# Kernel optimization log

Measured on AMD Instinct MI355X. Metric: run time of the kernel, lower is better.

## Reference

```python
import jax, jax.numpy as jnp
import numpy as np
import math

LEVEL_DIMS = [256, 512, 1024, 2048]
B, P, K, D = 8192, 64, 8, 512
EPS = 1e-5  # torch LayerNorm default eps


def _layernorm(x, g, b):
    m = jnp.mean(x, axis=-1, keepdims=True)
    v = jnp.var(x, axis=-1, keepdims=True)
    return (x - m) / jnp.sqrt(v + EPS) * g + b


def _l2norm(x):
    # F.normalize(dim=-1): x / max(||x||_2, 1e-12)
    n = jnp.sqrt(jnp.sum(x * x, axis=-1, keepdims=True))
    return x / jnp.maximum(n, 1e-12)


def setup_inputs() -> dict:
    key = jax.random.key(0)
    ks = iter(jax.random.split(key, 32))
    inp = {}
    for i, dim in enumerate(LEVEL_DIMS):
        inp[f'pooled_{i}'] = jax.random.normal(next(ks), (B, dim), jnp.float32)
        inp[f'proto_{i}'] = jax.random.normal(next(ks), (P, dim), jnp.float32)
        inp[f'ln_g_{i}'] = jnp.ones((2 * dim,), jnp.float32)
        inp[f'ln_b_{i}'] = jnp.zeros((2 * dim,), jnp.float32)
        inp[f'W_{i}'] = jax.random.normal(next(ks), (2 * dim, D), jnp.float32) * (1.0 / math.sqrt(2 * dim))
        inp[f'b_{i}'] = jnp.zeros((D,), jnp.float32)
    inp['text_base'] = jax.random.normal(next(ks), (K, D), jnp.float32)
    inp['logit_scale'] = jnp.ones((1,), jnp.float32)
    return inp


def reference(pooled_0, pooled_1, pooled_2, pooled_3,
              proto_0, proto_1, proto_2, proto_3,
              ln_g_0, ln_g_1, ln_g_2, ln_g_3,
              ln_b_0, ln_b_1, ln_b_2, ln_b_3,
              W_0, W_1, W_2, W_3,
              b_0, b_1, b_2, b_3,
              text_base, logit_scale):
    pooled = [pooled_0, pooled_1, pooled_2, pooled_3]
    proto = [proto_0, proto_1, proto_2, proto_3]
    ln_g = [ln_g_0, ln_g_1, ln_g_2, ln_g_3]
    ln_b = [ln_b_0, ln_b_1, ln_b_2, ln_b_3]
    Ws = [W_0, W_1, W_2, W_3]
    bs = [b_0, b_1, b_2, b_3]

    # text encoder: CLIP embeddings normalized, text_proj=Identity, normalized again (idempotent)
    text_features = _l2norm(text_base)  # [K, D]

    ctxs = []
    for pl, pr, g, bb, W, b in zip(pooled, proto, ln_g, ln_b, Ws, bs):
        proto_ctx = jnp.broadcast_to(jnp.mean(pr, axis=0, keepdims=True), pl.shape)  # [B, C]
        fused = jnp.concatenate([pl, proto_ctx], axis=1)  # [B, 2C]
        h = jax.nn.relu(_layernorm(fused, g, bb) @ W + b)  # [B, D]
        ctxs.append(_l2norm(h))
    image_contexts = jnp.stack(ctxs, axis=1)  # [B, L, D]

    logits = jnp.einsum('kd,bld->bkl', text_features, image_contexts)
    logits = logits / math.sqrt(D)
    logits = logits * jnp.clip(logit_scale, 1e-4, None)
    return jax.nn.softmax(logits, axis=-1)  # [B, K, L]
```

## Files before the change

kernel.cpp:

```cpp
#include <hip/hip_runtime.h>
#include <stdint.h>

typedef __bf16 bf16x8 __attribute__((ext_vector_type(8)));
typedef float f32x4 __attribute__((ext_vector_type(4)));

#define OFF_ABF   0u
#define OFF_GWT   62914560u
#define OFF_LOG   66846720u
#define OFF_STAT  100401152u
#define OFF_TEXT  100663296u
#define OFF_U     100679680u
#define OFF_GG    100687872u
#define OFF_BB    100696064u
#define OFF_SCAL  100704256u
#define WS_TOTAL  100719872u

__host__ __device__ __forceinline__ size_t abf_off(int l) {
  return (size_t)4194304u * (size_t)((1u << l) - 1u);
}
__host__ __device__ __forceinline__ size_t gwt_off(int l) {
  return (size_t)262144u * (size_t)((1u << l) - 1u);
}

__device__ __forceinline__ unsigned short f2bf(float x) {
  return (unsigned short)((__float_as_uint(x) + 0x8000u) >> 16);
}
__device__ __forceinline__ unsigned pack2(float a, float b) {
  return ((__float_as_uint(a) + 0x8000u) >> 16) |
         ((__float_as_uint(b) + 0x8000u) & 0xffff0000u);
}
__device__ __forceinline__ void async_load16(const void* g, void* l) {
  __builtin_amdgcn_global_load_lds((const __attribute__((address_space(1))) void*)g,
                                   (__attribute__((address_space(3))) void*)l,
                                   16, 0, 0);
}

struct PrepArgs {
  const float* pooled[4];
  const float* proto[4];
  const float* W[4];
  const float* g[4];
  const float* beta[4];
  const float* bias[4];
  const float* text;
  const float* lsc;
  char* ws;
};

__device__ __forceinline__ void loadUnit(f32x4 (&buf)[8], const f32x4* base, int lane) {
#pragma unroll
  for (int i = 0; i < 4; ++i) {
    buf[2 * i]     = base[2 * (lane + 64 * i)];
    buf[2 * i + 1] = base[2 * (lane + 64 * i) + 1];
  }
}

template <int R>
__device__ __forceinline__ void procUnit(const f32x4 (&v)[8], char* Dst, float* st,
                                         int rowBase, int lane) {
  float p1[4], p2[4];
#pragma unroll
  for (int i = 0; i < 4; ++i) {
    f32x4 a = v[2 * i], b = v[2 * i + 1];
    float s1 = ((a[0] + a[1]) + (a[2] + a[3])) + ((b[0] + b[1]) + (b[2] + b[3]));
    float s2 = 0.f;
    s2 = fmaf(a[0], a[0], s2); s2 = fmaf(a[1], a[1], s2);
    s2 = fmaf(a[2], a[2], s2); s2 = fmaf(a[3], a[3], s2);
    s2 = fmaf(b[0], b[0], s2); s2 = fmaf(b[1], b[1], s2);
    s2 = fmaf(b[2], b[2], s2); s2 = fmaf(b[3], b[3], s2);
    p1[i] = s1; p2[i] = s2;
    uint4 o = make_uint4(pack2(a[0], a[1]), pack2(a[2], a[3]),
                         pack2(b[0], b[1]), pack2(b[2], b[3]));
    *(uint4*)(Dst + 16 * (size_t)(lane + 64 * i)) = o;
  }
  if constexpr (R == 1) {
    float s1 = (p1[0] + p1[1]) + (p1[2] + p1[3]);
    float s2 = (p2[0] + p2[1]) + (p2[2] + p2[3]);
#pragma unroll
    for (int off = 1; off < 64; off <<= 1) {
      s1 += __shfl_xor(s1, off); s2 += __shfl_xor(s2, off);
    }
    if (lane == 0) {
      st[2 * (size_t)rowBase] = s1; st[2 * (size_t)rowBase + 1] = s2;
    }
  } else if constexpr (R == 2) {
#pragma unroll
    for (int h = 0; h < 2; ++h) {
      float s1 = p1[2 * h] + p1[2 * h + 1], s2 = p2[2 * h] + p2[2 * h + 1];
#pragma unroll
      for (int off = 1; off < 64; off <<= 1) {
        s1 += __shfl_xor(s1, off); s2 += __shfl_xor(s2, off);
      }
      if (lane == 0) {
        st[2 * (size_t)(rowBase + h)] = s1; st[2 * (size_t)(rowBase + h) + 1] = s2;
      }
    }
  } else if constexpr (R == 4) {
#pragma unroll
    for (int i = 0; i < 4; ++i) {
      float s1 = p1[i], s2 = p2[i];
#pragma unroll
      for (int off = 1; off < 64; off <<= 1) {
        s1 += __shfl_xor(s1, off); s2 += __shfl_xor(s2, off);
      }
      if (lane == 0) {
        st[2 * (size_t)(rowBase + i)] = s1; st[2 * (size_t)(rowBase + i) + 1] = s2;
      }
    }
  } else {
#pragma unroll
    for (int i = 0; i < 4; ++i) {
      float s1 = p1[i], s2 = p2[i];
#pragma unroll
      for (int off = 1; off < 32; off <<= 1) {
        s1 += __shfl_xor(s1, off); s2 += __shfl_xor(s2, off);
      }
      if ((lane & 31) == 0) {
        int row = rowBase + 2 * i + (lane >> 5);
        st[2 * (size_t)row] = s1; st[2 * (size_t)row + 1] = s2;
      }
    }
  }
}

__global__ __launch_bounds__(256, 4) void prep(PrepArgs A) {
  __shared__ unsigned short tile[128][66];
  __shared__ float redG[4][128], redB[4][128], redU[4][128];
  __shared__ float gsh[64], bsh[64], psh[64];
  __shared__ float redP[4][64];
  int t = threadIdx.x, bid = blockIdx.x;
  int w = t >> 6, lane = t & 63;

  if (bid >= 481) {
    int u0 = (bid - 481) * 4 + w;
    int l, uL;
    if (u0 < 8192)       { l = 3; uL = u0; }
    else if (u0 < 12288) { l = 2; uL = u0 - 8192; }
    else if (u0 < 14336) { l = 1; uL = u0 - 12288; }
    else                 { l = 0; uL = u0 - 14336; }
    const f32x4* P = (const f32x4*)A.pooled[l] + (size_t)uL * 512;
    char* Dst = A.ws + OFF_ABF + abf_off(l) + (size_t)uL * 4096;
    float* st = (float*)(A.ws + OFF_STAT) + (size_t)l * 8192 * 2;
    f32x4 v[8];
    loadUnit(v, P, lane);
    if (l == 3)      procUnit<1>(v, Dst, st, uL,     lane);
    else if (l == 2) procUnit<2>(v, Dst, st, uL * 2, lane);
    else if (l == 1) procUnit<4>(v, Dst, st, uL * 4, lane);
    else             procUnit<8>(v, Dst, st, uL * 8, lane);
    return;
  }

  if (bid == 480) {
    int row = t >> 5, l32 = t & 31;
    const float* tr = A.text + row * 512 + l32;
    float v[16];
    float s = 0.f;
#pragma unroll
    for (int i = 0; i < 16; ++i) {
      v[i] = tr[32 * i];
      s = fmaf(v[i], v[i], s);
    }
#pragma unroll
    for (int off = 1; off < 32; off <<= 1) s += __shfl_xor(s, off);
    float inv = 1.0f / fmaxf(sqrtf(s), 1e-12f);
    float* tf = (float*)(A.ws + OFF_TEXT) + row * 512 + l32;
#pragma unroll
    for (int i = 0; i < 16; ++i) tf[32 * i] = v[i] * inv;
    return;
  }

  int l, idl;
  if (bid < 256)      { l = 3; idl = bid; }
  else if (bid < 384) { l = 2; idl = bid - 256; }
  else if (bid < 448) { l = 1; idl = bid - 384; }
  else                { l = 0; idl = bid - 448; }
  int C = 256 << l;
  int sid = idl >> 2, dchunk = idl & 3;
  int j0 = sid * 64, d0 = dchunk * 128;
  bool top = (j0 < C);
  int L = lane;
  float* scal = (float*)(A.ws + OFF_SCAL);

  if (t < 64) {
    gsh[t] = A.g[l][j0 + t];
    bsh[t] = A.beta[l][j0 + t];
  }
  if (!top) {
    const float* pr = A.proto[l];
    int cb0 = j0 - C;
    float s = 0.f;
#pragma unroll
    for (int r = 0; r < 16; ++r) s += pr[(size_t)(w * 16 + r) * C + cb0 + L];
    redP[w][L] = s;
  }
  __syncthreads();
  if (!top) {
    if (t < 64) {
      float pmv = (redP[0][t] + redP[1][t] + redP[2][t] + redP[3][t]) * (1.0f / 64.0f);
      psh[t] = pmv * gsh[t];
      if (dchunk == 0) {
        float s1 = pmv, s2 = pmv * pmv;
#pragma unroll
        for (int off = 1; off < 64; off <<= 1) {
          s1 += __shfl_xor(s1, off);
          s2 += __shfl_xor(s2, off);
        }
        if (t == 0) {
          atomicAdd(&scal[l], s1);
          atomicAdd(&scal[4 + l], s2);
        }
      }
    }
    __syncthreads();
  }

  const float* W = A.W[l];
  float2 v[16];
#pragma unroll
  for (int r = 0; r < 16; ++r) {
    int j = j0 + w * 16 + r;
    v[r] = *(const float2*)(W + (size_t)j * 512 + d0 + 2 * L);
  }
  float gp0 = 0.f, gp1 = 0.f, bp0 = 0.f, bp1 = 0.f, up0 = 0.f, up1 = 0.f;
#pragma unroll
  for (int r = 0; r < 16; ++r) {
    int jl = w * 16 + r;
    float g = gsh[jl], b = bsh[jl];
    gp0 = fmaf(g, v[r].x, gp0); gp1 = fmaf(g, v[r].y, gp1);
    bp0 = fmaf(b, v[r].x, bp0); bp1 = fmaf(b, v[r].y, bp1);
    if (top) {
      tile[2 * L][jl] = f2bf(g * v[r].x);
      tile[2 * L + 1][jl] = f2bf(g * v[r].y);
    } else {
      float p = psh[jl];
      up0 = fmaf(p, v[r].x, up0); up1 = fmaf(p, v[r].y, up1);
    }
  }
  redG[w][2 * L] = gp0; redG[w][2 * L + 1] = gp1;
  redB[w][2 * L] = bp0; redB[w][2 * L + 1] = bp1;
  if (!top) { redU[w][2 * L] = up0; redU[w][2 * L + 1] = up1; }
  __syncthreads();

  if (t < 128) {
    int d = l * 512 + d0 + t;
    float G = redG[0][t] + redG[1][t] + redG[2][t] + redG[3][t];
    float B = redB[0][t] + redB[1][t] + redB[2][t] + redB[3][t];
    atomicAdd(&((float*)(A.ws + OFF_GG))[d], G);
    atomicAdd(&((float*)(A.ws + OFF_BB))[d], B);
    if (!top) {
      float U = redU[0][t] + redU[1][t] + redU[2][t] + redU[3][t];
      atomicAdd(&((float*)(A.ws + OFF_U))[d], U);
    }
  }
  if (top) {
    unsigned short* gwT = (unsigned short*)(A.ws + OFF_GWT + gwt_off(l));
    int d = t >> 1, jh = (t & 1) * 32;
    const unsigned* trow = (const unsigned*)&tile[d][jh];
    uint4 q0 = make_uint4(trow[0], trow[1], trow[2], trow[3]);
    uint4 q1 = make_uint4(trow[4], trow[5], trow[6], trow[7]);
    uint4 q2 = make_uint4(trow[8], trow[9], trow[10], trow[11]);
    uint4 q3 = make_uint4(trow[12], trow[13], trow[14], trow[15]);
    uint4* dst = (uint4*)(gwT + (size_t)(d0 + d) * C + j0 + jh);
    dst[0] = q0; dst[1] = q1; dst[2] = q2; dst[3] = q3;
  }
}

struct G2Args {
  char* ws;
  const float* bias[4];
};

__global__ __launch_bounds__(256, 4) void gemm2(G2Args A) {
  __shared__ __align__(16) char lds[39424];
  char* ws = A.ws;
  int t = threadIdx.x;
  int xcd = blockIdx.x & 7;
  int j   = blockIdx.x >> 3;
  int l   = 3 - (j >> 5);
  int jj  = j & 31;
  int rb  = xcd * 8 + (jj >> 2);
  int cb  = jj & 3;
  int C = 256 << l;
  int nst = C >> 5;
  int m0 = rb * 128, n0 = cb * 128;

  float* uArr  = (float*)(lds + 32768);
  float* gArr  = (float*)(lds + 33280);
  float* bArr  = (float*)(lds + 33792);
  float* rowM  = (float*)(lds + 34304);
  float* rowIS = (float*)(lds + 34816);
  float* textL = (float*)(lds + 35328);
  const float* scal = (const float*)(ws + OFF_SCAL);

  if (t < 128) {
    int idx = l * 512 + n0 + t;
    uArr[t] = ((const float*)(ws + OFF_U))[idx];
    gArr[t] = ((const float*)(ws + OFF_GG))[idx];
    bArr[t] = ((const float*)(ws + OFF_BB))[idx] + A.bias[l][n0 + t];
  } else {
    int r = t - 128;
    const float* st = (const float*)(ws + OFF_STAT) + (size_t)(l * 8192 + m0 + r) * 2;
    float s1 = st[0], s2 = st[1];
    float inv2C = 1.0f / (float)(2 * C);
    float mr = (s1 + scal[l]) * inv2C;
    float var = (s2 + scal[4 + l]) * inv2C - mr * mr;
    rowM[r] = mr;
    rowIS[r] = rsqrtf(var + 1e-5f);
  }
  {
    const float* tf = (const float*)(ws + OFF_TEXT);
#pragma unroll
    for (int i = 0; i < 4; ++i) {
      int idx = t + 256 * i;
      textL[idx] = tf[(idx >> 7) * 512 + n0 + (idx & 127)];
    }
  }

  int w = t >> 6, lane = t & 63, quad = lane >> 4, lc = lane & 15;
  const char* Abf = ws + OFF_ABF + abf_off(l);
  const char* Bw  = ws + OFF_GWT + gwt_off(l);
  const char* aP[2]; const char* bP[2];
  int aO[2], bO[2];
#pragma unroll
  for (int i = 0; i < 2; ++i) {
    int li = i * 256 + t;
    int rr = li >> 2, kq = li & 3;
    int sw = kq ^ ((rr >> 1) & 3);
    aP[i] = Abf + ((size_t)(m0 + rr) * C + sw * 8) * 2;
    bP[i] = Bw  + ((size_t)(n0 + rr) * C + sw * 8) * 2;
    aO[i] = i * 4096 + w * 1024;
    bO[i] = 8192 + i * 4096 + w * 1024;
  }
  int wr = (w >> 1) * 64, wc = (w & 1) * 64;
  int arow = wr + lc, brow = wc + lc;
  int aFo = arow * 64 + (quad ^ ((arow >> 1) & 3)) * 16;
  int bFo = 8192 + brow * 64 + (quad ^ ((brow >> 1) & 3)) * 16;

  async_load16(aP[0], lds + aO[0]); async_load16(aP[1], lds + aO[1]);
  async_load16(bP[0], lds + bO[0]); async_load16(bP[1], lds + bO[1]);
  aP[0] += 64; aP[1] += 64; bP[0] += 64; bP[1] += 64;
  __syncthreads();

  f32x4 acc[4][4] = {};
  for (int k = 0; k < nst; ++k) {
    int cur = k & 1;
    char* nb = lds + (cur ^ 1) * 16384;
    if (k + 1 < nst) {
      async_load16(aP[0], nb + aO[0]); async_load16(aP[1], nb + aO[1]);
      async_load16(bP[0], nb + bO[0]); async_load16(bP[1], nb + bO[1]);
      aP[0] += 64; aP[1] += 64; bP[0] += 64; bP[1] += 64;
    }
    const char* cbuf = lds + cur * 16384;
    const char* aF = cbuf + aFo;
    const char* bF = cbuf + bFo;
    bf16x8 av[4];
#pragma unroll
    for (int rt = 0; rt < 4; ++rt) av[rt] = *(const bf16x8*)(aF + rt * 1024);
#pragma unroll
    for (int ct = 0; ct < 4; ++ct) {
      bf16x8 bv = *(const bf16x8*)(bF + ct * 1024);
#pragma unroll
      for (int rt = 0; rt < 4; ++rt)
        acc[rt][ct] = __builtin_amdgcn_mfma_f32_16x16x32_bf16(av[rt], bv, acc[rt][ct], 0, 0, 0);
    }
    __syncthreads();
  }

  int slot = cb * 2 + (w & 1);
#pragma unroll
  for (int rt = 0; rt < 4; ++rt) {
#pragma unroll
    for (int reg = 0; reg < 4; ++reg) {
      int ml = wr + rt * 16 + quad * 4 + reg;
      float rm = rowM[ml], ris = rowIS[ml];
      float p[9] = {};
#pragma unroll
      for (int ct = 0; ct < 4; ++ct) {
        int nl = wc + ct * 16 + lc;
        float h = fmaf(acc[rt][ct][reg] + uArr[nl] - rm * gArr[nl], ris, bArr[nl]);
        h = fmaxf(h, 0.f);
        p[8] = fmaf(h, h, p[8]);
#pragma unroll
        for (int k = 0; k < 8; ++k)
          p[k] = fmaf(h, textL[k * 128 + nl], p[k]);
      }
#pragma unroll
      for (int off = 1; off < 16; off <<= 1) {
#pragma unroll
        for (int k = 0; k < 9; ++k) p[k] += __shfl_xor(p[k], off);
      }
      if (lc == 0) {
        float* Lg = (float*)(ws + OFF_LOG) +
                    ((((size_t)l * 8192 + m0 + ml) * 8 + slot) << 4);
#pragma unroll
        for (int k = 0; k < 9; ++k) Lg[k] = p[k];
      }
    }
  }
}

__global__ __launch_bounds__(256) void finishK(const char* ws, const float* lsc,
                                               float* out) {
  int t = threadIdx.x, wv = t >> 6, lane = t & 63;
  int row = blockIdx.x * 4 + wv;
  int s = lane >> 3, k = lane & 7;
  float scale = fmaxf(lsc[0], 1e-4f) * 0.04419417382415922f;
  float x[4];
#pragma unroll
  for (int l = 0; l < 4; ++l) {
    const float* Lg = (const float*)(ws + OFF_LOG) + (((size_t)l * 8192 + row) << 7);
    float d = Lg[s * 16 + k];
    float n = Lg[s * 16 + 8];
#pragma unroll
    for (int off = 8; off < 64; off <<= 1) {
      d += __shfl_xor(d, off);
      n += __shfl_xor(n, off);
    }
    x[l] = d * (scale / fmaxf(sqrtf(n), 1e-12f));
  }
  if (s == 0) {
    float mx = fmaxf(fmaxf(x[0], x[1]), fmaxf(x[2], x[3]));
    float e0 = __expf(x[0] - mx), e1 = __expf(x[1] - mx);
    float e2 = __expf(x[2] - mx), e3 = __expf(x[3] - mx);
    float inv = 1.0f / (e0 + e1 + e2 + e3);
    ((float4*)out)[(size_t)row * 8 + k] = make_float4(e0 * inv, e1 * inv, e2 * inv, e3 * inv);
  }
}

extern "C" void kernel_launch(void* const* d_in, const int* in_sizes, int n_in,
                              void* d_out, int out_size, void* d_ws, size_t ws_size,
                              hipStream_t stream) {
  (void)n_in; (void)out_size;
  if (ws_size < (size_t)WS_TOTAL) return;
  char* ws = (char*)d_ws;
  bool dict = (in_sizes[1] == 64 * 256);
  PrepArgs pa;
  for (int l = 0; l < 4; ++l) {
    if (dict) {
      pa.pooled[l] = (const float*)d_in[6 * l + 0];
      pa.proto[l]  = (const float*)d_in[6 * l + 1];
      pa.g[l]      = (const float*)d_in[6 * l + 2];
      pa.beta[l]   = (const float*)d_in[6 * l + 3];
      pa.W[l]      = (const float*)d_in[6 * l + 4];
      pa.bias[l]   = (const float*)d_in[6 * l + 5];
    } else {
      pa.pooled[l] = (const float*)d_in[l];
      pa.proto[l]  = (const float*)d_in[4 + l];
      pa.g[l]      = (const float*)d_in[8 + l];
      pa.beta[l]   = (const float*)d_in[12 + l];
      pa.W[l]      = (const float*)d_in[16 + l];
      pa.bias[l]   = (const float*)d_in[20 + l];
    }
  }
  pa.text = (const float*)d_in[24];
  pa.lsc = (const float*)d_in[25];
  pa.ws = ws;

  hipMemsetAsync(ws + OFF_U, 0, 3 * 8192 + 256, stream);

  prep<<<4321, 256, 0, stream>>>(pa);

  G2Args g2;
  g2.ws = ws;
  for (int l = 0; l < 4; ++l) g2.bias[l] = pa.bias[l];
  gemm2<<<1024, 256, 0, stream>>>(g2);
  finishK<<<2048, 256, 0, stream>>>(ws, pa.lsc, (float*)d_out);
}
```

Baseline: 277.4 us.

## Fuse pooled bf16 conversion and row stats into GEMM A-tile loading

Removes the prep-kernel stage that converted the pooled activations to bf16 in a workspace and computed per-row sum and sum-of-squares. The GEMM kernel now loads fp32 pooled rows directly from global memory into registers, packs them to bf16 in LDS with the same swizzle, and accumulates the row statistics on the fly. The LayerNorm mean and inverse std are reduced after the K loop. This avoids writing and re-reading about 60MB of bf16 workspace, at the cost of synchronous register-staged A loads, more register pressure (occupancy hint lowered to 3), and redundant fp32 reads of A by the four column blocks.

```diff
diff --git a/kernel.cpp b/kernel.cpp
--- a/kernel.cpp
+++ b/kernel.cpp
@@ -4,10 +4,8 @@
 typedef __bf16 bf16x8 __attribute__((ext_vector_type(8)));
 typedef float f32x4 __attribute__((ext_vector_type(4)));
 
-#define OFF_ABF   0u
 #define OFF_GWT   62914560u
 #define OFF_LOG   66846720u
-#define OFF_STAT  100401152u
 #define OFF_TEXT  100663296u
 #define OFF_U     100679680u
 #define OFF_GG    100687872u
@@ -15,9 +13,6 @@
 #define OFF_SCAL  100704256u
 #define WS_TOTAL  100719872u
 
-__host__ __device__ __forceinline__ size_t abf_off(int l) {
-  return (size_t)4194304u * (size_t)((1u << l) - 1u);
-}
 __host__ __device__ __forceinline__ size_t gwt_off(int l) {
   return (size_t)262144u * (size_t)((1u << l) - 1u);
 }
@@ -47,108 +42,13 @@
   char* ws;
 };
 
-__device__ __forceinline__ void loadUnit(f32x4 (&buf)[8], const f32x4* base, int lane) {
-#pragma unroll
-  for (int i = 0; i < 4; ++i) {
-    buf[2 * i]     = base[2 * (lane + 64 * i)];
-    buf[2 * i + 1] = base[2 * (lane + 64 * i) + 1];
-  }
-}
-
-template <int R>
-__device__ __forceinline__ void procUnit(const f32x4 (&v)[8], char* Dst, float* st,
-                                         int rowBase, int lane) {
-  float p1[4], p2[4];
-#pragma unroll
-  for (int i = 0; i < 4; ++i) {
-    f32x4 a = v[2 * i], b = v[2 * i + 1];
-    float s1 = ((a[0] + a[1]) + (a[2] + a[3])) + ((b[0] + b[1]) + (b[2] + b[3]));
-    float s2 = 0.f;
-    s2 = fmaf(a[0], a[0], s2); s2 = fmaf(a[1], a[1], s2);
-    s2 = fmaf(a[2], a[2], s2); s2 = fmaf(a[3], a[3], s2);
-    s2 = fmaf(b[0], b[0], s2); s2 = fmaf(b[1], b[1], s2);
-    s2 = fmaf(b[2], b[2], s2); s2 = fmaf(b[3], b[3], s2);
-    p1[i] = s1; p2[i] = s2;
-    uint4 o = make_uint4(pack2(a[0], a[1]), pack2(a[2], a[3]),
-                         pack2(b[0], b[1]), pack2(b[2], b[3]));
-    *(uint4*)(Dst + 16 * (size_t)(lane + 64 * i)) = o;
-  }
-  if constexpr (R == 1) {
-    float s1 = (p1[0] + p1[1]) + (p1[2] + p1[3]);
-    float s2 = (p2[0] + p2[1]) + (p2[2] + p2[3]);
-#pragma unroll
-    for (int off = 1; off < 64; off <<= 1) {
-      s1 += __shfl_xor(s1, off); s2 += __shfl_xor(s2, off);
-    }
-    if (lane == 0) {
-      st[2 * (size_t)rowBase] = s1; st[2 * (size_t)rowBase + 1] = s2;
-    }
-  } else if constexpr (R == 2) {
-#pragma unroll
-    for (int h = 0; h < 2; ++h) {
-      float s1 = p1[2 * h] + p1[2 * h + 1], s2 = p2[2 * h] + p2[2 * h + 1];
-#pragma unroll
-      for (int off = 1; off < 64; off <<= 1) {
-        s1 += __shfl_xor(s1, off); s2 += __shfl_xor(s2, off);
-      }
-      if (lane == 0) {
-        st[2 * (size_t)(rowBase + h)] = s1; st[2 * (size_t)(rowBase + h) + 1] = s2;
-      }
-    }
-  } else if constexpr (R == 4) {
-#pragma unroll
-    for (int i = 0; i < 4; ++i) {
-      float s1 = p1[i], s2 = p2[i];
-#pragma unroll
-      for (int off = 1; off < 64; off <<= 1) {
-        s1 += __shfl_xor(s1, off); s2 += __shfl_xor(s2, off);
-      }
-      if (lane == 0) {
-        st[2 * (size_t)(rowBase + i)] = s1; st[2 * (size_t)(rowBase + i) + 1] = s2;
-      }
-    }
-  } else {
-#pragma unroll
-    for (int i = 0; i < 4; ++i) {
-      float s1 = p1[i], s2 = p2[i];
-#pragma unroll
-      for (int off = 1; off < 32; off <<= 1) {
-        s1 += __shfl_xor(s1, off); s2 += __shfl_xor(s2, off);
-      }
-      if ((lane & 31) == 0) {
-        int row = rowBase + 2 * i + (lane >> 5);
-        st[2 * (size_t)row] = s1; st[2 * (size_t)row + 1] = s2;
-      }
-    }
-  }
-}
-
-__global__ __launch_bounds__(256, 4) void prep(PrepArgs A) {
+__global__ __launch_bounds__(256) void prep(PrepArgs A) {
   __shared__ unsigned short tile[128][66];
   __shared__ float redG[4][128], redB[4][128], redU[4][128];
   __shared__ float gsh[64], bsh[64], psh[64];
   __shared__ float redP[4][64];
   int t = threadIdx.x, bid = blockIdx.x;
   int w = t >> 6, lane = t & 63;
-
-  if (bid >= 481) {
-    int u0 = (bid - 481) * 4 + w;
-    int l, uL;
-    if (u0 < 8192)       { l = 3; uL = u0; }
-    else if (u0 < 12288) { l = 2; uL = u0 - 8192; }
-    else if (u0 < 14336) { l = 1; uL = u0 - 12288; }
-    else                 { l = 0; uL = u0 - 14336; }
-    const f32x4* P = (const f32x4*)A.pooled[l] + (size_t)uL * 512;
-    char* Dst = A.ws + OFF_ABF + abf_off(l) + (size_t)uL * 4096;
-    float* st = (float*)(A.ws + OFF_STAT) + (size_t)l * 8192 * 2;
-    f32x4 v[8];
-    loadUnit(v, P, lane);
-    if (l == 3)      procUnit<1>(v, Dst, st, uL,     lane);
-    else if (l == 2) procUnit<2>(v, Dst, st, uL * 2, lane);
-    else if (l == 1) procUnit<4>(v, Dst, st, uL * 4, lane);
-    else             procUnit<8>(v, Dst, st, uL * 8, lane);
-    return;
-  }
 
   if (bid == 480) {
     int row = t >> 5, l32 = t & 31;
@@ -267,10 +167,32 @@
 
 struct G2Args {
   char* ws;
+  const float* pooled[4];
   const float* bias[4];
 };
 
-__global__ __launch_bounds__(256, 4) void gemm2(G2Args A) {
+__device__ __forceinline__ void packStats(const f32x4& a0, const f32x4& a1,
+                                          const f32x4& a2, const f32x4& a3,
+                                          char* d0, char* d1,
+                                          float& s1a, float& s2a,
+                                          float& s1b, float& s2b) {
+  *(uint4*)d0 = make_uint4(pack2(a0[0], a0[1]), pack2(a0[2], a0[3]),
+                           pack2(a1[0], a1[1]), pack2(a1[2], a1[3]));
+  *(uint4*)d1 = make_uint4(pack2(a2[0], a2[1]), pack2(a2[2], a2[3]),
+                           pack2(a3[0], a3[1]), pack2(a3[2], a3[3]));
+  s1a += ((a0[0] + a0[1]) + (a0[2] + a0[3])) + ((a1[0] + a1[1]) + (a1[2] + a1[3]));
+  s2a = fmaf(a0[0], a0[0], s2a); s2a = fmaf(a0[1], a0[1], s2a);
+  s2a = fmaf(a0[2], a0[2], s2a); s2a = fmaf(a0[3], a0[3], s2a);
+  s2a = fmaf(a1[0], a1[0], s2a); s2a = fmaf(a1[1], a1[1], s2a);
+  s2a = fmaf(a1[2], a1[2], s2a); s2a = fmaf(a1[3], a1[3], s2a);
+  s1b += ((a2[0] + a2[1]) + (a2[2] + a2[3])) + ((a3[0] + a3[1]) + (a3[2] + a3[3]));
+  s2b = fmaf(a2[0], a2[0], s2b); s2b = fmaf(a2[1], a2[1], s2b);
+  s2b = fmaf(a2[2], a2[2], s2b); s2b = fmaf(a2[3], a2[3], s2b);
+  s2b = fmaf(a3[0], a3[0], s2b); s2b = fmaf(a3[1], a3[1], s2b);
+  s2b = fmaf(a3[2], a3[2], s2b); s2b = fmaf(a3[3], a3[3], s2b);
+}
+
+__global__ __launch_bounds__(256, 3) void gemm2(G2Args A) {
   __shared__ __align__(16) char lds[39424];
   char* ws = A.ws;
   int t = threadIdx.x;
@@ -297,15 +219,6 @@
     uArr[t] = ((const float*)(ws + OFF_U))[idx];
     gArr[t] = ((const float*)(ws + OFF_GG))[idx];
     bArr[t] = ((const float*)(ws + OFF_BB))[idx] + A.bias[l][n0 + t];
-  } else {
-    int r = t - 128;
-    const float* st = (const float*)(ws + OFF_STAT) + (size_t)(l * 8192 + m0 + r) * 2;
-    float s1 = st[0], s2 = st[1];
-    float inv2C = 1.0f / (float)(2 * C);
-    float mr = (s1 + scal[l]) * inv2C;
-    float var = (s2 + scal[4 + l]) * inv2C - mr * mr;
-    rowM[r] = mr;
-    rowIS[r] = rsqrtf(var + 1e-5f);
   }
   {
     const float* tf = (const float*)(ws + OFF_TEXT);
@@ -317,54 +230,106 @@
   }
 
   int w = t >> 6, lane = t & 63, quad = lane >> 4, lc = lane & 15;
-  const char* Abf = ws + OFF_ABF + abf_off(l);
-  const char* Bw  = ws + OFF_GWT + gwt_off(l);
-  const char* aP[2]; const char* bP[2];
-  int aO[2], bO[2];
+
+  int rA = t >> 2, sA = t & 3;
+  int gq = sA ^ ((rA >> 1) & 3);
+  const float* aG0 = A.pooled[l] + (size_t)(m0 + rA) * C + gq * 8;
+  const float* aG1 = aG0 + (size_t)64 * C;
+  char* aW0 = lds + (t << 4);
+  char* aW1 = aW0 + 4096;
+
+  const char* Bw = ws + OFF_GWT + gwt_off(l);
+  const char* bP[2]; int bO[2];
 #pragma unroll
   for (int i = 0; i < 2; ++i) {
     int li = i * 256 + t;
     int rr = li >> 2, kq = li & 3;
     int sw = kq ^ ((rr >> 1) & 3);
-    aP[i] = Abf + ((size_t)(m0 + rr) * C + sw * 8) * 2;
-    bP[i] = Bw  + ((size_t)(n0 + rr) * C + sw * 8) * 2;
-    aO[i] = i * 4096 + w * 1024;
-    bO[i] = 8192 + i * 4096 + w * 1024;
-  }
+    bP[i] = Bw + ((size_t)(n0 + rr) * C + sw * 8) * 2;
+    bO[i] = i * 4096 + w * 1024;
+  }
+
   int wr = (w >> 1) * 64, wc = (w & 1) * 64;
   int arow = wr + lc, brow = wc + lc;
   int aFo = arow * 64 + (quad ^ ((arow >> 1) & 3)) * 16;
-  int bFo = 8192 + brow * 64 + (quad ^ ((brow >> 1) & 3)) * 16;
-
-  async_load16(aP[0], lds + aO[0]); async_load16(aP[1], lds + aO[1]);
-  async_load16(bP[0], lds + bO[0]); async_load16(bP[1], lds + bO[1]);
-  aP[0] += 64; aP[1] += 64; bP[0] += 64; bP[1] += 64;
-  __syncthreads();
+  int bFo = brow * 64 + (quad ^ ((brow >> 1) & 3)) * 16;
 
   f32x4 acc[4][4] = {};
-  for (int k = 0; k < nst; ++k) {
-    int cur = k & 1;
-    char* nb = lds + (cur ^ 1) * 16384;
-    if (k + 1 < nst) {
-      async_load16(aP[0], nb + aO[0]); async_load16(aP[1], nb + aO[1]);
-      async_load16(bP[0], nb + bO[0]); async_load16(bP[1], nb + bO[1]);
-      aP[0] += 64; aP[1] += 64; bP[0] += 64; bP[1] += 64;
-    }
-    const char* cbuf = lds + cur * 16384;
-    const char* aF = cbuf + aFo;
-    const char* bF = cbuf + bFo;
+  float s1a = 0.f, s2a = 0.f, s1b = 0.f, s2b = 0.f;
+  f32x4 e0, e1, e2, e3, o0, o1, o2, o3;
+
+  auto mfmaStep = [&](const char* ab, const char* bb) {
     bf16x8 av[4];
 #pragma unroll
-    for (int rt = 0; rt < 4; ++rt) av[rt] = *(const bf16x8*)(aF + rt * 1024);
+    for (int rt = 0; rt < 4; ++rt) av[rt] = *(const bf16x8*)(ab + aFo + rt * 1024);
 #pragma unroll
     for (int ct = 0; ct < 4; ++ct) {
-      bf16x8 bv = *(const bf16x8*)(bF + ct * 1024);
+      bf16x8 bv = *(const bf16x8*)(bb + bFo + ct * 1024);
 #pragma unroll
       for (int rt = 0; rt < 4; ++rt)
         acc[rt][ct] = __builtin_amdgcn_mfma_f32_16x16x32_bf16(av[rt], bv, acc[rt][ct], 0, 0, 0);
     }
+  };
+
+  e0 = *(const f32x4*)aG0; e1 = *(const f32x4*)(aG0 + 4);
+  e2 = *(const f32x4*)aG1; e3 = *(const f32x4*)(aG1 + 4);
+  aG0 += 32; aG1 += 32;
+  async_load16(bP[0], lds + 16384 + bO[0]);
+  async_load16(bP[1], lds + 16384 + bO[1]);
+  bP[0] += 64; bP[1] += 64;
+  packStats(e0, e1, e2, e3, aW0, aW1, s1a, s2a, s1b, s2b);
+  o0 = *(const f32x4*)aG0; o1 = *(const f32x4*)(aG0 + 4);
+  o2 = *(const f32x4*)aG1; o3 = *(const f32x4*)(aG1 + 4);
+  aG0 += 32; aG1 += 32;
+  __syncthreads();
+
+  for (int k = 0; k < nst; k += 2) {
+    if (k + 1 < nst) {
+      async_load16(bP[0], lds + 24576 + bO[0]);
+      async_load16(bP[1], lds + 24576 + bO[1]);
+      bP[0] += 64; bP[1] += 64;
+      packStats(o0, o1, o2, o3, lds + 8192 + (t << 4), lds + 8192 + 4096 + (t << 4),
+                s1a, s2a, s1b, s2b);
+      if (k + 2 < nst) {
+        e0 = *(const f32x4*)aG0; e1 = *(const f32x4*)(aG0 + 4);
+        e2 = *(const f32x4*)aG1; e3 = *(const f32x4*)(aG1 + 4);
+        aG0 += 32; aG1 += 32;
+      }
+    }
+    mfmaStep(lds, lds + 16384);
     __syncthreads();
-  }
+    if (k + 1 >= nst) break;
+    if (k + 2 < nst) {
+      async_load16(bP[0], lds + 16384 + bO[0]);
+      async_load16(bP[1], lds + 16384 + bO[1]);
+      bP[0] += 64; bP[1] += 64;
+      packStats(e0, e1, e2, e3, aW0, aW1, s1a, s2a, s1b, s2b);
+      if (k + 3 < nst) {
+        o0 = *(const f32x4*)aG0; o1 = *(const f32x4*)(aG0 + 4);
+        o2 = *(const f32x4*)aG1; o3 = *(const f32x4*)(aG1 + 4);
+        aG0 += 32; aG1 += 32;
+      }
+    }
+    mfmaStep(lds + 8192, lds + 24576);
+    __syncthreads();
+  }
+
+#pragma unroll
+  for (int off = 1; off < 4; off <<= 1) {
+    s1a += __shfl_xor(s1a, off); s2a += __shfl_xor(s2a, off);
+    s1b += __shfl_xor(s1b, off); s2b += __shfl_xor(s2b, off);
+  }
+  if ((t & 3) == 0) {
+    float inv2C = 1.0f / (float)(2 * C);
+    float spro = scal[l], sqpro = scal[4 + l];
+    float mra = (s1a + spro) * inv2C;
+    rowM[rA] = mra;
+    rowIS[rA] = rsqrtf((s2a + sqpro) * inv2C - mra * mra + 1e-5f);
+    float mrb = (s1b + spro) * inv2C;
+    rowM[64 + rA] = mrb;
+    rowIS[64 + rA] = rsqrtf((s2b + sqpro) * inv2C - mrb * mrb + 1e-5f);
+  }
+  __syncthreads();
 
   int slot = cb * 2 + (w & 1);
 #pragma unroll
@@ -458,11 +423,14 @@
 
   hipMemsetAsync(ws + OFF_U, 0, 3 * 8192 + 256, stream);
 
-  prep<<<4321, 256, 0, stream>>>(pa);
+  prep<<<481, 256, 0, stream>>>(pa);
 
   G2Args g2;
   g2.ws = ws;
-  for (int l = 0; l < 4; ++l) g2.bias[l] = pa.bias[l];
+  for (int l = 0; l < 4; ++l) {
+    g2.pooled[l] = pa.pooled[l];
+    g2.bias[l] = pa.bias[l];
+  }
   gemm2<<<1024, 256, 0, stream>>>(g2);
   finishK<<<2048, 256, 0, stream>>>(ws, pa.lsc, (float*)d_out);
 }
```

Measured after the change: 267.3 us. -3.6%, faster.
